# Performance work log

Hardware: AMD Instinct MI355X
Metric: run time of the kernel (lower is better)

The kernel has to match this reference:

```python
import jax, jax.numpy as jnp
import numpy as np
from jax import lax

FILTERS = [(1, 32), (2, 32), (3, 64), (4, 128), (5, 256), (6, 512), (7, 1024)]
CHAR_VOCAB, CHAR_DIM, MAX_CHARS = 262, 16, 50
N_FILTERS = sum(n for _, n in FILTERS)  # 2048
PROJ_DIM = 512
B, S = 16, 256


def setup_inputs() -> dict:
    key = jax.random.key(0)
    ks = jax.random.split(key, 32)
    inp = {}
    inp["words"] = jax.random.randint(ks[0], (B, S), 0, 50000)
    inp["chars"] = jax.random.randint(ks[1], (B, S, MAX_CHARS), 0, CHAR_VOCAB)
    inp["char_emb"] = jax.random.normal(ks[2], (CHAR_VOCAB, CHAR_DIM), jnp.float32) * 0.1
    for i, (w, n) in enumerate(FILTERS):
        inp[f"conv_w_{i}"] = jax.random.normal(ks[3 + i], (n, CHAR_DIM, w), jnp.float32) * 0.1
        inp[f"conv_b_{i}"] = jnp.zeros((n,), jnp.float32)
    for j in range(2):
        inp[f"hw_w_{j}"] = jax.random.normal(ks[12 + j], (2 * N_FILTERS, N_FILTERS), jnp.float32) * 0.02
        # Highway init: transform bias = 0, gate bias = 1
        inp[f"hw_b_{j}"] = jnp.concatenate([jnp.zeros((N_FILTERS,), jnp.float32), jnp.ones((N_FILTERS,), jnp.float32)])
    inp["proj_w"] = jax.random.normal(ks[20], (PROJ_DIM, N_FILTERS), jnp.float32) * 0.02
    inp["proj_b"] = jnp.zeros((PROJ_DIM,), jnp.float32)
    return inp


def _char_cnn(chars, char_emb, conv_ws, conv_bs, hw_ws, hw_bs, proj_w, proj_b):
    b, s, L = chars.shape
    # (B*S, CHAR_DIM, L)
    x = char_emb[chars].reshape(b * s, L, -1).transpose(0, 2, 1)
    convs = []
    for w, bias in zip(conv_ws, conv_bs):
        # Conv1d valid, NCW layout; y: (N, num, L-width+1)
        y = lax.conv_general_dilated(x, w, (1,), "VALID", dimension_numbers=("NCH", "OIH", "NCH"))
        y = y + bias[None, :, None]
        y = jnp.max(y, axis=-1)          # max over time
        convs.append(jax.nn.relu(y))      # activation
    h = jnp.concatenate(convs, axis=-1)   # (N, 2048)
    d = h.shape[-1]
    for W, bb in zip(hw_ws, hw_bs):
        p = h @ W.T + bb
        nonlinear = jax.nn.relu(p[:, :d])
        gate = jax.nn.sigmoid(p[:, d:])
        h = gate * h + (1.0 - gate) * nonlinear
    out = h @ proj_w.T + proj_b
    return out.reshape(b, s, -1)


def reference(words, chars, char_emb,
              conv_w_0, conv_b_0, conv_w_1, conv_b_1, conv_w_2, conv_b_2,
              conv_w_3, conv_b_3, conv_w_4, conv_b_4, conv_w_5, conv_b_5,
              conv_w_6, conv_b_6, hw_w_0, hw_b_0, hw_w_1, hw_b_1, proj_w, proj_b):
    conv_ws = [conv_w_0, conv_w_1, conv_w_2, conv_w_3, conv_w_4, conv_w_5, conv_w_6]
    conv_bs = [conv_b_0, conv_b_1, conv_b_2, conv_b_3, conv_b_4, conv_b_5, conv_b_6]
    return _char_cnn(chars, char_emb, conv_ws, conv_bs, [hw_w_0, hw_w_1], [hw_b_0, hw_b_1], proj_w, proj_b)
```

## Files before the change

### kernel.cpp

```cpp
#include <hip/hip_runtime.h>
#include <hip/hip_bf16.h>


#define NTOK 4096
#define NF   2048
#define KDIM 2048
#define HID  4096
#define PDIM 512

typedef __attribute__((ext_vector_type(4))) float floatx4;
typedef __attribute__((ext_vector_type(8))) short shortx8;

__device__ inline void async_copy16(const void* g, void* l) {
  __builtin_amdgcn_global_load_lds(
      (const __attribute__((address_space(1))) void*)(uintptr_t)g,
      (__attribute__((address_space(3))) void*)(uint32_t)(uintptr_t)l,
      16, 0, 0);
}

__device__ inline void bar() {
  __builtin_amdgcn_sched_barrier(0);
  __builtin_amdgcn_s_barrier();
  __builtin_amdgcn_sched_barrier(0);
}

#define WAITCNT_VM(N)                                  \
  do {                                                 \
    __builtin_amdgcn_sched_barrier(0);                 \
    asm volatile("s_waitcnt vmcnt(" #N ")");           \
    __builtin_amdgcn_sched_barrier(0);                 \
  } while (0)

__global__ __launch_bounds__(256) void cvt8_kernel(
    const float* __restrict__ s, __hip_bfloat16* __restrict__ d, int n8) {
  int i = blockIdx.x * 256 + threadIdx.x;
  if (i < n8) {
    floatx4 v0 = *(const floatx4*)(s + (size_t)i * 8);
    floatx4 v1 = *(const floatx4*)(s + (size_t)i * 8 + 4);
    union { shortx8 v; __hip_bfloat16 h[8]; } u;
#pragma unroll
    for (int t = 0; t < 4; ++t) u.h[t] = __float2bfloat16(v0[t]);
#pragma unroll
    for (int t = 0; t < 4; ++t) u.h[4 + t] = __float2bfloat16(v1[t]);
    *(shortx8*)(d + (size_t)i * 8) = u.v;
  }
}

__global__ __launch_bounds__(256) void cvt_hw8(
    const float* __restrict__ s, __hip_bfloat16* __restrict__ d) {
  int i = blockIdx.x * 256 + threadIdx.x;
  int r = i >> 8;
  int kb = (i & 255) * 8;
  int sr = (r >> 1) + (r & 1) * 2048;
  const float* src = s + (size_t)sr * 2048 + kb;
  floatx4 v0 = *(const floatx4*)(src);
  floatx4 v1 = *(const floatx4*)(src + 4);
  union { shortx8 v; __hip_bfloat16 h[8]; } u;
#pragma unroll
  for (int t = 0; t < 4; ++t) u.h[t] = __float2bfloat16(v0[t]);
#pragma unroll
  for (int t = 0; t < 4; ++t) u.h[4 + t] = __float2bfloat16(v1[t]);
  *(shortx8*)(d + (size_t)r * 2048 + kb) = u.v;
}

__global__ __launch_bounds__(256) void conv_wprep(
    const float* __restrict__ w0, const float* __restrict__ w1,
    const float* __restrict__ w2, const float* __restrict__ w3,
    const float* __restrict__ w4, const float* __restrict__ w5,
    const float* __restrict__ w6,
    const float* __restrict__ b0, const float* __restrict__ b1,
    const float* __restrict__ b2, const float* __restrict__ b3,
    const float* __restrict__ b4, const float* __restrict__ b5,
    const float* __restrict__ b6, const float* __restrict__ emb,
    __hip_bfloat16* __restrict__ Wb, float* __restrict__ Bc,
    __hip_bfloat16* __restrict__ embb) {
  int idx = blockIdx.x * 256 + threadIdx.x;
  const int start[7] = {0, 32, 64, 128, 256, 512, 1024};
  const float* ws[7] = {w0, w1, w2, w3, w4, w5, w6};
  const float* bs[7] = {b0, b1, b2, b3, b4, b5, b6};
  if (idx < 262144) {
    int ch = idx >> 7, kp = idx & 127;
    int f = (ch >= 32) + (ch >= 64) + (ch >= 128) + (ch >= 256) +
            (ch >= 512) + (ch >= 1024);
    int w = f + 1, lc = ch - start[f];
    int d = kp & 15, k = kp >> 4;
    float v = (k < w) ? ws[f][((size_t)lc * 16 + d) * w + k] : 0.f;
    Wb[idx] = __float2bfloat16(v);
  } else if (idx < 262144 + 2048) {
    int ch = idx - 262144;
    int f = (ch >= 32) + (ch >= 64) + (ch >= 128) + (ch >= 256) +
            (ch >= 512) + (ch >= 1024);
    Bc[ch] = bs[f][ch - start[f]];
  } else if (idx < 262144 + 2048 + 4192) {
    int e = idx - 262144 - 2048;
    embb[e] = __float2bfloat16(emb[e]);
  }
}

template <int NKT, int NT, int ROWS>
__global__ __launch_bounds__(256) void conv_k(
    const int* __restrict__ chars, const __hip_bfloat16* __restrict__ embb,
    const __hip_bfloat16* __restrict__ Wb, const float* __restrict__ bias,
    __hip_bfloat16* __restrict__ h, int chbase) {
  __shared__ __align__(16) __hip_bfloat16 Xs[2 * 4 * ROWS * 24];
  int tid = threadIdx.x, wave = tid >> 6, lane = tid & 63;
  int frow = lane & 15, q = lane >> 4;
  int chb = chbase + blockIdx.y * 64;
  int tokbase = blockIdx.x * 32;

  shortx8 wreg[NKT][4];
#pragma unroll
  for (int kt = 0; kt < NKT; ++kt)
#pragma unroll
    for (int j = 0; j < 4; ++j)
      wreg[kt][j] = *(const shortx8*)(
          Wb + (size_t)(chb + j * 16 + frow) * 128 + kt * 32 + q * 8);

  float blane = bias[chb + lane];
  int Tvj[4];
#pragma unroll
  for (int j = 0; j < 4; ++j) {
    int ch = chb + j * 16 + frow;
    int w = 1 + (ch >= 32) + (ch >= 64) + (ch >= 128) + (ch >= 256) +
            (ch >= 512) + (ch >= 1024);
    Tvj[j] = 51 - w;
  }

  auto stage = [&](int g, int buf) {
    constexpr int NST = 4 * ROWS;
#pragma unroll
    for (int rep = 0; rep < (NST + 255) / 256; ++rep) {
      int rr = tid + rep * 256;
      if (rr < NST) {
        int tk = rr / ROWS, r = rr - tk * ROWS;
        __hip_bfloat16* dst = Xs + ((size_t)(buf * 4 + tk) * ROWS + r) * 24;
        if (r < 50) {
          int c = chars[(size_t)(tokbase + g * 4 + tk) * 50 + r];
          const shortx8* e = (const shortx8*)(embb + c * 16);
          *(shortx8*)(dst) = e[0];
          *(shortx8*)(dst + 8) = e[1];
        } else if (g <= 1) {
          shortx8 z = {0, 0, 0, 0, 0, 0, 0, 0};
          *(shortx8*)(dst) = z;
          *(shortx8*)(dst + 8) = z;
        }
      }
    }
  };

  stage(0, 0);
  __syncthreads();

  const floatx4 zero = {0.f, 0.f, 0.f, 0.f};
#pragma unroll 1
  for (int g = 0; g < 8; ++g) {
    if (g < 7) stage(g + 1, (g + 1) & 1);

    const __hip_bfloat16* Xw = Xs + (size_t)((g & 1) * 4 + wave) * ROWS * 24;
    floatx4 acc[NT][4];

#pragma unroll
    for (int kt = 0; kt < NKT; ++kt) {
      int kk = kt * 2 + (q >> 1);
      int d0 = (q & 1) * 8;
      shortx8 xf[NT];
#pragma unroll
      for (int i = 0; i < NT; ++i)
        xf[i] = *(const shortx8*)(Xw + (i * 16 + frow + kk) * 24 + d0);
#pragma unroll
      for (int i = 0; i < NT; ++i)
#pragma unroll
        for (int j = 0; j < 4; ++j) {
          if (kt == 0)
            acc[i][j] = __builtin_amdgcn_mfma_f32_16x16x32_bf16(
                xf[i], wreg[0][j], zero, 0, 0, 0);
          else
            acc[i][j] = __builtin_amdgcn_mfma_f32_16x16x32_bf16(
                xf[i], wreg[kt][j], acc[i][j], 0, 0, 0);
        }
    }

    float vj[4];
#pragma unroll
    for (int j = 0; j < 4; ++j) {
      float v = -1e30f;
#pragma unroll
      for (int i = 0; i < NT; ++i) {
#pragma unroll
        for (int r = 0; r < 4; ++r) {
          if (i < 2) {
            v = fmaxf(v, acc[i][j][r]);
          } else {
            int t = i * 16 + q * 4 + r;
            if (t < Tvj[j]) v = fmaxf(v, acc[i][j][r]);
          }
        }
      }
      v = fmaxf(v, __shfl_xor(v, 16));
      v = fmaxf(v, __shfl_xor(v, 32));
      vj[j] = v;
    }
    float r0 = (q & 2) ? vj[2] : vj[0];
    float r1 = (q & 2) ? vj[3] : vj[1];
    float rv = (q & 1) ? r1 : r0;
    int tok = tokbase + g * 4 + wave;
    h[(size_t)tok * NF + chb + lane] =
        __float2bfloat16(fmaxf(rv + blane, 0.f));
    __syncthreads();
  }
}

__global__ __launch_bounds__(512, 2) void gemm_hw8(
    const __hip_bfloat16* __restrict__ A, const __hip_bfloat16* __restrict__ B,
    const float* __restrict__ hwb, __hip_bfloat16* __restrict__ Hdst) {
  __shared__ __align__(16) __hip_bfloat16 As[2 * 256 * 64];
  __shared__ __align__(16) __hip_bfloat16 Bs[2 * 256 * 64];
  int tid = threadIdx.x;
  int wave = tid >> 6, lane = tid & 63;
  int wr = wave >> 2, wc = wave & 3;
  int sr8 = lane >> 3, sc8 = lane & 7;
  int frow = lane & 15, q = lane >> 4;

  int wg = blockIdx.x;
  int swz = (wg & 7) * 32 + (wg >> 3);
  int bm = swz & 15;
  int bn = swz >> 4;

  const __hip_bfloat16* Ab = A + (size_t)bn * 256 * KDIM;
  const __hip_bfloat16* Bb = B + (size_t)bm * 256 * KDIM;

  floatx4 acc[8][4];
  const floatx4 zero = {0.f, 0.f, 0.f, 0.f};
#pragma unroll
  for (int i = 0; i < 8; ++i)
#pragma unroll
    for (int j = 0; j < 4; ++j) acc[i][j] = zero;

  auto stage_half = [&](const __hip_bfloat16* gsrc, __hip_bfloat16* lbase,
                        int d, int hf, int kb) {
#pragma unroll
    for (int it = 0; it < 2; ++it) {
      int row = hf * 128 + (wave * 2 + it) * 8;
      int r = row + sr8;
      int gc = sc8 ^ sr8;
      async_copy16(gsrc + (size_t)r * KDIM + kb + gc * 8,
                   (char*)lbase + ((size_t)d * 256 + row) * 128);
    }
  };

  auto lda2 = [&](shortx8* dst2, const __hip_bfloat16* Asd, int i0, int s) {
#pragma unroll
    for (int ii = 0; ii < 2; ++ii) {
      int r = wr * 128 + (i0 + ii) * 16 + frow;
      dst2[ii] = *(const shortx8*)(Asd + r * 64 +
                                   (((s * 4 + q) ^ (frow & 7)) << 3));
    }
  };
  auto ldb4 = [&](shortx8* dst4, const __hip_bfloat16* Bsd, int s) {
#pragma unroll
    for (int j = 0; j < 4; ++j) {
      int r = wc * 64 + j * 16 + frow;
      dst4[j] = *(const shortx8*)(Bsd + r * 64 +
                                  (((s * 4 + q) ^ (frow & 7)) << 3));
    }
  };
  auto mma8 = [&](const shortx8* aX, const shortx8* bX, int i0) {
    __builtin_amdgcn_s_setprio(1);
#pragma unroll
    for (int ii = 0; ii < 2; ++ii)
#pragma unroll
      for (int j = 0; j < 4; ++j)
        acc[i0 + ii][j] = __builtin_amdgcn_mfma_f32_16x16x32_bf16(
            aX[ii], bX[j], acc[i0 + ii][j], 0, 0, 0);
    __builtin_amdgcn_s_setprio(0);
  };

  stage_half(Ab, As, 0, 0, 0);
  stage_half(Ab, As, 0, 1, 0);
  stage_half(Bb, Bs, 0, 0, 0);
  stage_half(Bb, Bs, 0, 1, 0);
  stage_half(Bb, Bs, 1, 0, 64);
  stage_half(Bb, Bs, 1, 1, 64);
  WAITCNT_VM(4);
  bar();

  const int NTILE = KDIM / 64;
#pragma unroll 2
  for (int T = 0; T < NTILE; ++T) {
    int d = T & 1, d1 = d ^ 1;
    const __hip_bfloat16* Asd = As + d * 16384;
    const __hip_bfloat16* Bsd = Bs + d * 16384;
    int kn = (T + 1) * 64;

    shortx8 aU[2], aV[2], b0[4], b1[4];
    ldb4(b0, Bsd, 0);
    lda2(aU, Asd, 0, 0);
    if (T + 1 < NTILE) {
      stage_half(Ab, As, d1, 0, kn);
      stage_half(Ab, As, d1, 1, kn);
    }
    lda2(aV, Asd, 2, 0);
    mma8(aU, b0, 0);
    lda2(aU, Asd, 4, 0);
    mma8(aV, b0, 2);
    lda2(aV, Asd, 6, 0);
    ldb4(b1, Bsd, 1);
    mma8(aU, b0, 4);
    lda2(aU, Asd, 0, 1);
    mma8(aV, b0, 6);
    lda2(aV, Asd, 2, 1);
    mma8(aU, b1, 0);
    bar();
    if (T + 2 < NTILE) stage_half(Bb, Bs, d, 0, kn + 64);
    lda2(aU, Asd, 4, 1);
    mma8(aV, b1, 2);
    if (T + 2 < NTILE) stage_half(Bb, Bs, d, 1, kn + 64);
    lda2(aV, Asd, 6, 1);
    mma8(aU, b1, 4);
    mma8(aV, b1, 6);
    if (T + 2 < NTILE) {
      WAITCNT_VM(4);
    } else if (T + 1 < NTILE) {
      WAITCNT_VM(0);
    }
    bar();
  }

  int crow0 = bn * 256 + wr * 128 + q * 4;
  int ccol0 = bm * 256 + wc * 64 + frow;
#pragma unroll
  for (int i = 0; i < 8; ++i)
#pragma unroll
    for (int j = 0; j < 4; ++j) {
      int gcol = ccol0 + j * 16;
      float bb = (gcol & 1) ? hwb[2048 + (gcol >> 1)] : hwb[gcol >> 1];
#pragma unroll
      for (int r = 0; r < 4; ++r) {
        int row = crow0 + i * 16 + r;
        float v = acc[i][j][r] + bb;
        float partner = __shfl_xor(v, 1);
        if (!(lane & 1)) {
          float gte = 1.f / (1.f + expf(-partner));
          int ch = gcol >> 1;
          float hold = __bfloat162float(A[(size_t)row * 2048 + ch]);
          float hnew = gte * hold + (1.f - gte) * fmaxf(v, 0.f);
          Hdst[(size_t)row * 2048 + ch] = __float2bfloat16(hnew);
        }
      }
    }
}

__global__ __launch_bounds__(256) void gemm_proj(
    const __hip_bfloat16* __restrict__ A, const __hip_bfloat16* __restrict__ B,
    float* __restrict__ C, const float* __restrict__ bias) {
  const int K = KDIM;
  __shared__ __align__(16) __hip_bfloat16 As[32 * 64];
  __shared__ __align__(16) __hip_bfloat16 Bs[128 * 64];
  int tid = threadIdx.x;
  int wave = tid >> 6, lane = tid & 63;
  int wr = wave >> 1, wc = wave & 1;
  int bn = blockIdx.y, bm = blockIdx.x;

  int sr8 = lane >> 3, sc8 = lane & 7;
  int frow = lane & 15, q = lane >> 4;

  floatx4 acc[4];
  floatx4 zero = {0.f, 0.f, 0.f, 0.f};
#pragma unroll
  for (int j = 0; j < 4; ++j) acc[j] = zero;

  const __hip_bfloat16* Ab = A + (size_t)bn * 32 * K;
  const __hip_bfloat16* Bb = B + (size_t)bm * 128 * K;

  for (int kb = 0; kb < K; kb += 64) {
    __syncthreads();
    {
      int r = wave * 8 + sr8;
      int gc = sc8 ^ (r & 7);
      async_copy16(Ab + (size_t)r * K + kb + gc * 8, (char*)As + wave * 1024);
    }
#pragma unroll
    for (int it = 0; it < 4; ++it) {
      int seg = wave * 4 + it;
      int r = seg * 8 + sr8;
      int gc = sc8 ^ (r & 7);
      async_copy16(Bb + (size_t)r * K + kb + gc * 8, (char*)Bs + seg * 1024);
    }
    __syncthreads();

#pragma unroll
    for (int s = 0; s < 2; ++s) {
      shortx8 af, bf[4];
      {
        int r = wr * 16 + frow;
        af = *(const shortx8*)(As + r * 64 + ((s * 4 + q) ^ (r & 7)) * 8);
      }
#pragma unroll
      for (int j = 0; j < 4; ++j) {
        int r = wc * 64 + j * 16 + frow;
        bf[j] = *(const shortx8*)(Bs + r * 64 + ((s * 4 + q) ^ (r & 7)) * 8);
      }
#pragma unroll
      for (int j = 0; j < 4; ++j)
        acc[j] = __builtin_amdgcn_mfma_f32_16x16x32_bf16(af, bf[j], acc[j],
                                                          0, 0, 0);
    }
  }

  int crow0 = bn * 32 + wr * 16 + q * 4;
  int ccol0 = bm * 128 + wc * 64 + frow;
#pragma unroll
  for (int j = 0; j < 4; ++j) {
    int c = ccol0 + j * 16;
#pragma unroll
    for (int r = 0; r < 4; ++r) {
      int row = crow0 + r;
      C[(size_t)row * PDIM + c] = acc[j][r] + bias[c];
    }
  }
}

extern "C" void kernel_launch(void* const* d_in, const int* in_sizes, int n_in,
                              void* d_out, int out_size, void* d_ws, size_t ws_size,
                              hipStream_t stream) {
  const int*   chars  = (const int*)d_in[1];
  const float* emb    = (const float*)d_in[2];
  const float* cw[7];
  const float* cb[7];
  for (int i = 0; i < 7; ++i) {
    cw[i] = (const float*)d_in[3 + 2 * i];
    cb[i] = (const float*)d_in[4 + 2 * i];
  }
  const float* hw_w0  = (const float*)d_in[17];
  const float* hw_b0  = (const float*)d_in[18];
  const float* hw_w1  = (const float*)d_in[19];
  const float* hw_b1  = (const float*)d_in[20];
  const float* proj_w = (const float*)d_in[21];
  const float* proj_b = (const float*)d_in[22];
  float* out = (float*)d_out;

  char* ws = (char*)d_ws;
  __hip_bfloat16* h      = (__hip_bfloat16*)(ws);
  __hip_bfloat16* h2     = (__hip_bfloat16*)(ws + (16ull << 20));
  __hip_bfloat16* convWb = (__hip_bfloat16*)(ws + (32ull << 20));
  float*          convBc = (float*)(ws + (32ull << 20) + 524288);
  __hip_bfloat16* embb   = (__hip_bfloat16*)(ws + (32ull << 20) + 524288 + 8192);
  __hip_bfloat16* w0b    = (__hip_bfloat16*)(ws + (48ull << 20));
  __hip_bfloat16* w1b    = (__hip_bfloat16*)(ws + (64ull << 20));
  __hip_bfloat16* pwb    = (__hip_bfloat16*)(ws + (80ull << 20));

  cvt_hw8<<<(HID * KDIM / 8) / 256, 256, 0, stream>>>(hw_w0, w0b);
  cvt_hw8<<<(HID * KDIM / 8) / 256, 256, 0, stream>>>(hw_w1, w1b);
  cvt8_kernel<<<(PDIM * KDIM / 8) / 256, 256, 0, stream>>>(proj_w, pwb,
                                                           PDIM * KDIM / 8);
  conv_wprep<<<(262144 + 2048 + 4192 + 255) / 256, 256, 0, stream>>>(
      cw[0], cw[1], cw[2], cw[3], cw[4], cw[5], cw[6],
      cb[0], cb[1], cb[2], cb[3], cb[4], cb[5], cb[6], emb,
      convWb, convBc, embb);

  conv_k<1, 4, 72><<<dim3(128, 1), 256, 0, stream>>>(chars, embb, convWb,
                                                     convBc, h, 0);
  conv_k<2, 3, 56><<<dim3(128, 3), 256, 0, stream>>>(chars, embb, convWb,
                                                     convBc, h, 64);
  conv_k<3, 3, 56><<<dim3(128, 12), 256, 0, stream>>>(chars, embb, convWb,
                                                      convBc, h, 256);
  conv_k<4, 3, 56><<<dim3(128, 16), 256, 0, stream>>>(chars, embb, convWb,
                                                      convBc, h, 1024);

  gemm_hw8<<<dim3(256), 512, 0, stream>>>(h, w0b, hw_b0, h2);
  gemm_hw8<<<dim3(256), 512, 0, stream>>>(h2, w1b, hw_b1, h);
  gemm_proj<<<dim3(PDIM / 128, NTOK / 32), 256, 0, stream>>>(h, pwb, out,
                                                             proj_b);
}
```

Before: 456.2 us.

## Merge conv launches into one kernel and gather embeddings directly without LDS

The four templated conv launches become a single conv_all launch that dispatches on blockIdx.y to the right width specialization. The LDS double-buffered staging of embedded characters and its per-step __syncthreads are removed. Each wave instead loads its token's char ids into lanes, broadcasts them with __shfl, and reads the bf16 embedding rows straight from global memory (a 8KB table that stays in cache). This cuts launch overhead, tail effects and barrier cost, at the price of redundant global/L1 loads per MFMA fragment and a mixed-workload grid.

```diff
diff --git a/kernel.cpp b/kernel.cpp
--- a/kernel.cpp
+++ b/kernel.cpp
@@ -97,16 +97,13 @@
   }
 }
 
-template <int NKT, int NT, int ROWS>
-__global__ __launch_bounds__(256) void conv_k(
+template <int NKT, int NT>
+__device__ __forceinline__ void conv_body(
     const int* __restrict__ chars, const __hip_bfloat16* __restrict__ embb,
     const __hip_bfloat16* __restrict__ Wb, const float* __restrict__ bias,
-    __hip_bfloat16* __restrict__ h, int chbase) {
-  __shared__ __align__(16) __hip_bfloat16 Xs[2 * 4 * ROWS * 24];
+    __hip_bfloat16* __restrict__ h, int chb, int tokbase) {
   int tid = threadIdx.x, wave = tid >> 6, lane = tid & 63;
   int frow = lane & 15, q = lane >> 4;
-  int chb = chbase + blockIdx.y * 64;
-  int tokbase = blockIdx.x * 32;
 
   shortx8 wreg[NKT][4];
 #pragma unroll
@@ -126,47 +123,27 @@
     Tvj[j] = 51 - w;
   }
 
-  auto stage = [&](int g, int buf) {
-    constexpr int NST = 4 * ROWS;
-#pragma unroll
-    for (int rep = 0; rep < (NST + 255) / 256; ++rep) {
-      int rr = tid + rep * 256;
-      if (rr < NST) {
-        int tk = rr / ROWS, r = rr - tk * ROWS;
-        __hip_bfloat16* dst = Xs + ((size_t)(buf * 4 + tk) * ROWS + r) * 24;
-        if (r < 50) {
-          int c = chars[(size_t)(tokbase + g * 4 + tk) * 50 + r];
-          const shortx8* e = (const shortx8*)(embb + c * 16);
-          *(shortx8*)(dst) = e[0];
-          *(shortx8*)(dst + 8) = e[1];
-        } else if (g <= 1) {
-          shortx8 z = {0, 0, 0, 0, 0, 0, 0, 0};
-          *(shortx8*)(dst) = z;
-          *(shortx8*)(dst + 8) = z;
-        }
-      }
-    }
-  };
-
-  stage(0, 0);
-  __syncthreads();
-
   const floatx4 zero = {0.f, 0.f, 0.f, 0.f};
+  int kkb = q >> 1, d0 = (q & 1) * 8;
+
 #pragma unroll 1
   for (int g = 0; g < 8; ++g) {
-    if (g < 7) stage(g + 1, (g + 1) & 1);
-
-    const __hip_bfloat16* Xw = Xs + (size_t)((g & 1) * 4 + wave) * ROWS * 24;
+    int tok = tokbase + g * 4 + wave;
+    int crow = (lane < 50) ? chars[(size_t)tok * 50 + lane] : 0;
+
     floatx4 acc[NT][4];
-
 #pragma unroll
     for (int kt = 0; kt < NKT; ++kt) {
-      int kk = kt * 2 + (q >> 1);
-      int d0 = (q & 1) * 8;
+      int kk = kt * 2 + kkb;
       shortx8 xf[NT];
 #pragma unroll
-      for (int i = 0; i < NT; ++i)
-        xf[i] = *(const shortx8*)(Xw + (i * 16 + frow + kk) * 24 + d0);
+      for (int i = 0; i < NT; ++i) {
+        int tp = i * 16 + frow + kk;
+        int c = __shfl(crow, tp & 63);
+        shortx8 xv = {0, 0, 0, 0, 0, 0, 0, 0};
+        if (tp < 50) xv = *(const shortx8*)(embb + c * 16 + d0);
+        xf[i] = xv;
+      }
 #pragma unroll
       for (int i = 0; i < NT; ++i)
 #pragma unroll
@@ -203,11 +180,26 @@
     float r0 = (q & 2) ? vj[2] : vj[0];
     float r1 = (q & 2) ? vj[3] : vj[1];
     float rv = (q & 1) ? r1 : r0;
-    int tok = tokbase + g * 4 + wave;
     h[(size_t)tok * NF + chb + lane] =
         __float2bfloat16(fmaxf(rv + blane, 0.f));
-    __syncthreads();
-  }
+  }
+}
+
+__global__ __launch_bounds__(256) void conv_all(
+    const int* __restrict__ chars, const __hip_bfloat16* __restrict__ embb,
+    const __hip_bfloat16* __restrict__ Wb, const float* __restrict__ bias,
+    __hip_bfloat16* __restrict__ h) {
+  int by = blockIdx.y;
+  int chb = by * 64;
+  int tokbase = blockIdx.x * 32;
+  if (by == 0)
+    conv_body<1, 4>(chars, embb, Wb, bias, h, chb, tokbase);
+  else if (by < 4)
+    conv_body<2, 3>(chars, embb, Wb, bias, h, chb, tokbase);
+  else if (by < 16)
+    conv_body<3, 3>(chars, embb, Wb, bias, h, chb, tokbase);
+  else
+    conv_body<4, 3>(chars, embb, Wb, bias, h, chb, tokbase);
 }
 
 __global__ __launch_bounds__(512, 2) void gemm_hw8(
@@ -458,14 +450,7 @@
       cb[0], cb[1], cb[2], cb[3], cb[4], cb[5], cb[6], emb,
       convWb, convBc, embb);
 
-  conv_k<1, 4, 72><<<dim3(128, 1), 256, 0, stream>>>(chars, embb, convWb,
-                                                     convBc, h, 0);
-  conv_k<2, 3, 56><<<dim3(128, 3), 256, 0, stream>>>(chars, embb, convWb,
-                                                     convBc, h, 64);
-  conv_k<3, 3, 56><<<dim3(128, 12), 256, 0, stream>>>(chars, embb, convWb,
-                                                      convBc, h, 256);
-  conv_k<4, 3, 56><<<dim3(128, 16), 256, 0, stream>>>(chars, embb, convWb,
-                                                      convBc, h, 1024);
+  conv_all<<<dim3(128, 32), 256, 0, stream>>>(chars, embb, convWb, convBc, h);
 
   gemm_hw8<<<dim3(256), 512, 0, stream>>>(h, w0b, hw_b0, h2);
   gemm_hw8<<<dim3(256), 512, 0, stream>>>(h2, w1b, hw_b1, h);
```

New measurement: 466.3 us. +2.2%, slower.
